# Kernel optimization log

Hardware: AMD Instinct MI355X
Metric: run time of the kernel (lower is better)

The kernel has to match this reference:

```python
import jax, jax.numpy as jnp
import numpy as np
from jax import lax

B, C, H, W = 64, 512, 14, 14
HEAD_DIM = 32
NUM_HEADS = C // HEAD_DIM
HIDDEN = int(C * 4.0)
EPS = 1e-5
LS_INIT = 1e-5


def setup_inputs() -> dict:
    key = jax.random.key(0)
    ks = jax.random.split(key, 16)
    d = {}
    d['x'] = jax.random.normal(ks[0], (B, C, H, W), dtype=jnp.float32)
    # shared BatchNorm2d(dim) (inference-mode, running stats)
    d['bn_g'] = 1.0 + 0.1 * jax.random.normal(ks[1], (C,), dtype=jnp.float32)
    d['bn_b'] = 0.1 * jax.random.normal(ks[2], (C,), dtype=jnp.float32)
    d['bn_m'] = 0.1 * jax.random.normal(ks[3], (C,), dtype=jnp.float32)
    d['bn_v'] = jax.random.uniform(ks[4], (C,), minval=0.5, maxval=1.5, dtype=jnp.float32)
    # MHSA params (qkv_bias=False)
    d['qkv_w'] = 0.02 * jax.random.normal(ks[5], (3 * C, C), dtype=jnp.float32)
    d['proj_w'] = 0.02 * jax.random.normal(ks[6], (C, C), dtype=jnp.float32)
    d['proj_b'] = jnp.zeros((C,), dtype=jnp.float32)
    # ConvFFN: depthwise 7x7 (groups=C, no bias) -> BN -> 1x1 -> GELU -> 1x1
    d['dw_w'] = 0.02 * jax.random.normal(ks[7], (C, 1, 7, 7), dtype=jnp.float32)
    d['fbn_g'] = 1.0 + 0.1 * jax.random.normal(ks[8], (C,), dtype=jnp.float32)
    d['fbn_b'] = 0.1 * jax.random.normal(ks[9], (C,), dtype=jnp.float32)
    d['fbn_m'] = 0.1 * jax.random.normal(ks[10], (C,), dtype=jnp.float32)
    d['fbn_v'] = jax.random.uniform(ks[11], (C,), minval=0.5, maxval=1.5, dtype=jnp.float32)
    d['fc1_w'] = 0.02 * jax.random.normal(ks[12], (HIDDEN, C), dtype=jnp.float32)
    d['fc1_b'] = jnp.zeros((HIDDEN,), dtype=jnp.float32)
    d['fc2_w'] = 0.02 * jax.random.normal(ks[13], (C, HIDDEN), dtype=jnp.float32)
    d['fc2_b'] = jnp.zeros((C,), dtype=jnp.float32)
    # layer scale params, shape (C,1,1)
    d['ls1'] = LS_INIT * jnp.ones((C, 1, 1), dtype=jnp.float32)
    d['ls2'] = LS_INIT * jnp.ones((C, 1, 1), dtype=jnp.float32)
    return d


def _bn2d(x, g, b, m, v):
    # inference BatchNorm2d over channel dim of NCHW
    inv = g * lax.rsqrt(v + EPS)
    return x * inv[None, :, None, None] + (b - m * inv)[None, :, None, None]


def _mhsa(x, qkv_w, proj_w, proj_b):
    b, c, h, w = x.shape
    n = h * w
    xt = x.reshape(b, c, n).transpose(0, 2, 1)              # [B,N,C]
    qkv = xt @ qkv_w.T                                       # [B,N,3C]
    qkv = qkv.reshape(b, n, 3, NUM_HEADS, HEAD_DIM).transpose(2, 0, 3, 1, 4)
    q, k, v = qkv[0], qkv[1], qkv[2]                         # [B,h,N,d]
    scale = HEAD_DIM ** -0.5
    attn = jax.nn.softmax(jnp.einsum('bhnd,bhmd->bhnm', q * scale, k), axis=-1)
    o = jnp.einsum('bhnm,bhmd->bhnd', attn, v)               # [B,h,N,d]
    o = o.transpose(0, 2, 1, 3).reshape(b, n, c)             # [B,N,C]
    o = o @ proj_w.T + proj_b
    return o.transpose(0, 2, 1).reshape(b, c, h, w)


def _convffn(x, dw_w, fbn_g, fbn_b, fbn_m, fbn_v, fc1_w, fc1_b, fc2_w, fc2_b):
    y = lax.conv_general_dilated(x, dw_w, window_strides=(1, 1),
                                 padding=[(3, 3), (3, 3)],
                                 feature_group_count=C,
                                 dimension_numbers=('NCHW', 'OIHW', 'NCHW'))
    y = _bn2d(y, fbn_g, fbn_b, fbn_m, fbn_v)
    y = jnp.einsum('bchw,oc->bohw', y, fc1_w) + fc1_b[None, :, None, None]
    y = jax.nn.gelu(y, approximate=False)
    y = jnp.einsum('bchw,oc->bohw', y, fc2_w) + fc2_b[None, :, None, None]
    return y


def reference(x, bn_g, bn_b, bn_m, bn_v, qkv_w, proj_w, proj_b,
              dw_w, fbn_g, fbn_b, fbn_m, fbn_v, fc1_w, fc1_b, fc2_w, fc2_b,
              ls1, ls2):
    xn = _bn2d(x, bn_g, bn_b, bn_m, bn_v)
    x = x + ls1[None] * _mhsa(xn, qkv_w, proj_w, proj_b)
    xn = _bn2d(x, bn_g, bn_b, bn_m, bn_v)
    x = x + ls2[None] * _convffn(xn, dw_w, fbn_g, fbn_b, fbn_m, fbn_v,
                                 fc1_w, fc1_b, fc2_w, fc2_b)
    return x
```

## Files before the change

### kernel.cpp

```cpp
#include <hip/hip_runtime.h>
#include <hip/hip_bf16.h>
#include <hip/hip_fp8.h>
#include <stdint.h>

#define NTOK 196
#define NB   64
#define CCH  512
#define HID  2048
#define MTOT (NB * NTOK)

typedef __attribute__((ext_vector_type(8))) short  short8v;
typedef __attribute__((ext_vector_type(4))) float  float4v;
typedef __attribute__((ext_vector_type(2))) int    int2v;


__device__ __forceinline__ void mfma16x16(float4v& d, short8v a, short8v b) {
  asm("v_mfma_f32_16x16x32_bf16 %0, %1, %2, %0" : "+v"(d) : "v"(a), "v"(b));
}

__device__ __forceinline__ void mfma_fp8(float4v& d, int2v a, int2v b) {
  asm("v_mfma_f32_16x16x32_fp8_fp8 %0, %1, %2, %0" : "+v"(d) : "v"(a), "v"(b));
}

__device__ __forceinline__ void gload_lds16(const void* gsrc, void* ldst) {
  __builtin_amdgcn_global_load_lds(
      (const __attribute__((address_space(1))) unsigned int*)gsrc,
      (__attribute__((address_space(3))) unsigned int*)ldst, 16, 0, 0);
}

__device__ __forceinline__ int swz4(int r) { return (r ^ (r >> 2)) & 3; }

__device__ __forceinline__ uint8_t to_fp8(float v) {
  return __hip_fp8_e4m3(v).__x;
}


__global__ void prep_consts(const float* __restrict__ bn_g, const float* __restrict__ bn_b,
                            const float* __restrict__ bn_m, const float* __restrict__ bn_v,
                            const float* __restrict__ fbn_g, const float* __restrict__ fbn_b,
                            const float* __restrict__ fbn_m, const float* __restrict__ fbn_v,
                            float* __restrict__ cst) {
  int c = blockIdx.x * blockDim.x + threadIdx.x;
  if (c < CCH) {
    float i1 = bn_g[c] * rsqrtf(bn_v[c] + 1e-5f);
    cst[c] = i1;
    cst[512 + c] = bn_b[c] - bn_m[c] * i1;
    float i2 = fbn_g[c] * rsqrtf(fbn_v[c] + 1e-5f);
    cst[1024 + c] = i2;
    cst[1536 + c] = fbn_b[c] - fbn_m[c] * i2;
  }
}


__global__ void cvt_weights(const float* __restrict__ qkv_w, const float* __restrict__ proj_w,
                            const float* __restrict__ fc1_w, const float* __restrict__ fc2_w,
                            uint8_t* __restrict__ qkvb, uint8_t* __restrict__ projb,
                            uint8_t* __restrict__ fc1b, uint8_t* __restrict__ fc2b) {
  int i4 = blockIdx.x * blockDim.x + threadIdx.x;
  const int nq = 1536 * 512 / 4;
  const int np = 512 * 512 / 4;
  const int n1 = 2048 * 512 / 4;
  const float* src;
  uint8_t* dst;
  int k;
  if (i4 < nq)                { src = qkv_w;  dst = qkvb;  k = i4; }
  else if (i4 < nq + np)      { src = proj_w; dst = projb; k = i4 - nq; }
  else if (i4 < nq + np + n1) { src = fc1_w;  dst = fc1b;  k = i4 - nq - np; }
  else                        { src = fc2_w;  dst = fc2b;  k = i4 - nq - np - n1; }
  float4v v = *(const float4v*)(src + 4 * (size_t)k);
  #pragma unroll
  for (int l = 0; l < 4; ++l) dst[4 * (size_t)k + l] = to_fp8(v[l] * 16.0f);
}


__global__ __launch_bounds__(256) void transpose_x(
    const float* __restrict__ x, uint8_t* __restrict__ xnt8,
    __hip_bfloat16* __restrict__ xt, const float* __restrict__ cst) {
  __shared__ float tile[32][33];
  const int n0 = blockIdx.x * 32;
  const int c0 = blockIdx.y * 32;
  const int b  = blockIdx.z;
  const int j = threadIdx.x & 31, i = threadIdx.x >> 5;
  #pragma unroll
  for (int p = 0; p < 4; ++p) {
    int cc = c0 + i + p * 8;
    int n = n0 + j;
    if (n < NTOK) tile[i + p * 8][j] = x[((size_t)b * CCH + cc) * NTOK + n];
  }
  __syncthreads();
  const float s = cst[c0 + j], t = cst[512 + c0 + j];
  #pragma unroll
  for (int p = 0; p < 4; ++p) {
    int n = n0 + i + p * 8;
    int cc = c0 + j;
    if (n < NTOK) {
      float raw = tile[j][i + p * 8];
      size_t o = ((size_t)b * NTOK + n) * CCH + cc;
      xt[o]   = __float2bfloat16(raw);
      xnt8[o] = to_fp8(raw * s + t);
    }
  }
}


template<int EPI>
__global__ __launch_bounds__(256, 3) void gemm8f(
    const uint8_t* __restrict__ A, const uint8_t* __restrict__ Bw,
    int N, int K, int NY,
    __hip_bfloat16* __restrict__ outb, uint8_t* __restrict__ out8,
    float* __restrict__ outf,
    const float* __restrict__ bias, const float* __restrict__ ls,
    const __hip_bfloat16* __restrict__ resid) {
  __shared__ char lds[49152];
  const int tid  = threadIdx.x;
  const int lane = tid & 63;
  const int wave = tid >> 6;

  const int q    = (int)gridDim.x >> 3;
  const int orig = blockIdx.x;
  const int wgid = (orig & 7) * q + (orig >> 3);
  const int bx = wgid / NY;
  const int by = wgid - bx * NY;

  const int m0 = bx * 128;
  const int n0 = by * 128;
  const int wm = (wave >> 1) * 64;
  const int wn = (wave & 1) * 64;
  const int KT = K >> 6;

  float4v acc[4][4] = {};

  auto stage = [&](int buf, int kt) {
    const int kb = kt * 64;
    char* base = lds + buf * 16384;
    #pragma unroll
    for (int i = 0; i < 2; ++i) {
      int L = i * 4096 + tid * 16;
      int row = L >> 6;
      int lc = ((L >> 4) & 3) ^ swz4(row);
      gload_lds16(A + (size_t)(m0 + row) * K + kb + lc * 16, base + L);
    }
    #pragma unroll
    for (int i = 0; i < 2; ++i) {
      int L = i * 4096 + tid * 16;
      int row = L >> 6;
      int lc = ((L >> 4) & 3) ^ swz4(row);
      gload_lds16(Bw + (size_t)(n0 + row) * K + kb + lc * 16, base + 8192 + L);
    }
  };

  auto compute = [&](int buf) {
    const char* bA = lds + buf * 16384;
    const char* bB = bA + 8192;
    const int g = lane >> 4;
    #pragma unroll
    for (int t = 0; t < 2; ++t) {
      int2v av[4], bv[4];
      #pragma unroll
      for (int f = 0; f < 4; ++f) {
        int row = wm + f * 16 + (lane & 15);
        int c16 = ((t << 1) | (g >> 1)) ^ swz4(row);
        av[f] = *(const int2v*)(bA + row * 64 + c16 * 16 + (g & 1) * 8);
      }
      #pragma unroll
      for (int j = 0; j < 4; ++j) {
        int row = wn + j * 16 + (lane & 15);
        int c16 = ((t << 1) | (g >> 1)) ^ swz4(row);
        bv[j] = *(const int2v*)(bB + row * 64 + c16 * 16 + (g & 1) * 8);
      }
      #pragma unroll
      for (int i = 0; i < 4; ++i)
        #pragma unroll
        for (int j = 0; j < 4; ++j)
          mfma_fp8(acc[i][j], av[i], bv[j]);
    }
  };

  stage(0, 0);
  stage(1, 1);
  int cur = 0;
  for (int kt = 0; kt < KT - 1; ++kt) {
    asm volatile("s_waitcnt vmcnt(4)" ::: "memory");
    __builtin_amdgcn_s_barrier();
    __builtin_amdgcn_sched_barrier(0);
    if (kt + 2 < KT) {
      int s = cur + 2; if (s >= 3) s -= 3;
      stage(s, kt + 2);
    }
    compute(cur);
    ++cur; if (cur == 3) cur = 0;
  }
  asm volatile("s_waitcnt vmcnt(0)" ::: "memory");
  __builtin_amdgcn_s_barrier();
  __builtin_amdgcn_sched_barrier(0);
  compute(cur);
  asm volatile("s_nop 7\n\ts_nop 7");

  const float RS = 0.0625f;

  if (EPI == 0 || EPI == 2) {
    #pragma unroll
    for (int i = 0; i < 4; ++i)
      #pragma unroll
      for (int j = 0; j < 4; ++j)
        #pragma unroll
        for (int r = 0; r < 4; ++r) {
          int m = m0 + wm + i * 16 + ((lane >> 4) << 2) + r;
          int n = n0 + wn + j * 16 + (lane & 15);
          float v = acc[i][j][r] * RS;
          if (EPI == 0) {
            outb[(size_t)m * N + n] = __float2bfloat16(v);
          } else {
            float z = v + bias[n];
            float g2 = z / (1.0f + __expf(-1.702f * z));
            out8[(size_t)m * N + n] = to_fp8(g2);
          }
        }
  } else if (EPI == 1) {
    #pragma unroll
    for (int i = 0; i < 4; ++i)
      #pragma unroll
      for (int j = 0; j < 4; ++j)
        #pragma unroll
        for (int r = 0; r < 4; ++r) {
          int m = m0 + wm + i * 16 + ((lane >> 4) << 2) + r;
          int n = n0 + wn + j * 16 + (lane & 15);
          float v = acc[i][j][r] * RS + bias[n];
          v = __bfloat162float(resid[(size_t)m * CCH + n]) + ls[n] * v;
          outb[(size_t)m * CCH + n] = __float2bfloat16(v);
        }
  } else {
    float* LT = (float*)lds;
    #pragma unroll 1
    for (int hh = 0; hh < 2; ++hh) {
      __syncthreads();
      if ((wn >> 6) == hh) {
        #pragma unroll
        for (int i = 0; i < 4; ++i)
          #pragma unroll
          for (int j = 0; j < 4; ++j)
            #pragma unroll
            for (int r = 0; r < 4; ++r) {
              int ml = wm + i * 16 + ((lane >> 4) << 2) + r;
              int nl = j * 16 + (lane & 15);
              int n = n0 + wn + nl;
              float v = acc[i][j][r] * RS + bias[n];
              v = __bfloat162float(resid[(size_t)(m0 + ml) * CCH + n]) + ls[n] * v;
              LT[nl * 129 + ml] = v;
            }
      }
      __syncthreads();
      {
        int ml0 = lane << 1;
        int mg = m0 + ml0;
        int bb0 = mg / NTOK;
        int tt0 = mg - bb0 * NTOK;
        int bb1 = (mg + 1) / NTOK;
        int tt1 = (mg + 1) - bb1 * NTOK;
        size_t base0 = (size_t)bb0 * (CCH * NTOK) + tt0;
        size_t base1 = (size_t)bb1 * (CCH * NTOK) + tt1;
        #pragma unroll
        for (int u = 0; u < 16; ++u) {
          int cr = wave * 16 + u;
          int cg = n0 + hh * 64 + cr;
          float v0 = LT[cr * 129 + ml0];
          float v1 = LT[cr * 129 + ml0 + 1];
          outf[base0 + (size_t)cg * NTOK] = v0;
          outf[base1 + (size_t)cg * NTOK] = v1;
        }
      }
    }
  }
}


__global__ __launch_bounds__(256, 2) void attn_kernel(
    const __hip_bfloat16* __restrict__ qkv, uint8_t* __restrict__ o_t8) {
  __shared__ char sQ[208 * 64];
  __shared__ char sK[224 * 64];
  __shared__ char sV[32 * 448];
  __shared__ char sP[4][16 * 472];
  const int tid  = threadIdx.x;
  const int lane = tid & 63;
  const int wave = tid >> 6;
  const int b = blockIdx.x >> 4;
  const int h = blockIdx.x & 15;
  const size_t qbase = (size_t)b * NTOK * 1536 + h * 32;

  {
    uint32_t* z = (uint32_t*)sQ;
    for (int i = tid; i < (208 * 64) / 4; i += 256) z[i] = 0u;
    z = (uint32_t*)sK;
    for (int i = tid; i < (224 * 64) / 4; i += 256) z[i] = 0u;
    z = (uint32_t*)sV;
    for (int i = tid; i < (32 * 448) / 4; i += 256) z[i] = 0u;
  }
  __syncthreads();

  for (int p = tid; p < NTOK * 4; p += 256) {
    int row = p >> 2, c = p & 3;
    const __hip_bfloat16* src = qkv + qbase + (size_t)row * 1536 + c * 8;
    short8v q = *(const short8v*)(src);
    short8v k = *(const short8v*)(src + 512);
    short8v v = *(const short8v*)(src + 1024);
    int pc = c ^ swz4(row);
    *(short8v*)(sQ + row * 64 + pc * 16) = q;
    *(short8v*)(sK + row * 64 + pc * 16) = k;
    #pragma unroll
    for (int j = 0; j < 8; ++j) {
      int d = c * 8 + j;
      int ch = (row >> 3) ^ swz4(d);
      *(uint16_t*)(sV + d * 448 + ch * 16 + (row & 7) * 2) = (uint16_t)v[j];
    }
  }
  __syncthreads();

  const float scale = 0.17677669529663687f;
  char* Pw = sP[wave];

  for (int mt = wave; mt < 13; mt += 4) {
    int qrow = mt * 16 + (lane & 15);
    int pcq = (lane >> 4) ^ swz4(qrow);
    short8v aq = *(const short8v*)(sQ + qrow * 64 + pcq * 16);

    float4v s[14];
    #pragma unroll
    for (int nt = 0; nt < 14; ++nt) {
      int krow = nt * 16 + (lane & 15);
      int pck = (lane >> 4) ^ swz4(krow);
      short8v bk = *(const short8v*)(sK + krow * 64 + pck * 16);
      s[nt] = float4v{0.f, 0.f, 0.f, 0.f};
      mfma16x16(s[nt], aq, bk);
    }
    asm volatile("s_nop 7\n\ts_nop 7");

    float mx[4] = {-INFINITY, -INFINITY, -INFINITY, -INFINITY};
    #pragma unroll
    for (int nt = 0; nt < 14; ++nt) {
      bool valid = (nt * 16 + (lane & 15)) < NTOK;
      #pragma unroll
      for (int r = 0; r < 4; ++r) {
        float v = valid ? s[nt][r] * scale : -INFINITY;
        s[nt][r] = v;
        mx[r] = fmaxf(mx[r], v);
      }
    }
    #pragma unroll
    for (int off = 1; off < 16; off <<= 1) {
      #pragma unroll
      for (int r = 0; r < 4; ++r) mx[r] = fmaxf(mx[r], __shfl_xor(mx[r], off));
    }
    float sum[4] = {0.f, 0.f, 0.f, 0.f};
    #pragma unroll
    for (int nt = 0; nt < 14; ++nt) {
      #pragma unroll
      for (int r = 0; r < 4; ++r) {
        float e = __expf(s[nt][r] - mx[r]);
        s[nt][r] = e;
        sum[r] += e;
      }
    }
    #pragma unroll
    for (int off = 1; off < 16; off <<= 1) {
      #pragma unroll
      for (int r = 0; r < 4; ++r) sum[r] += __shfl_xor(sum[r], off);
    }
    float rs[4];
    #pragma unroll
    for (int r = 0; r < 4; ++r) rs[r] = 1.0f / sum[r];

    #pragma unroll
    for (int nt = 0; nt < 14; ++nt) {
      int col = nt * 16 + (lane & 15);
      #pragma unroll
      for (int r = 0; r < 4; ++r) {
        int prow = ((lane >> 4) << 2) + r;
        *(__hip_bfloat16*)(Pw + prow * 472 + col * 2) = __float2bfloat16(s[nt][r] * rs[r]);
      }
    }

    float4v o0 = float4v{0.f, 0.f, 0.f, 0.f};
    float4v o1 = float4v{0.f, 0.f, 0.f, 0.f};
    #pragma unroll
    for (int ks = 0; ks < 7; ++ks) {
      short8v pa = *(const short8v*)(Pw + (lane & 15) * 472 + ks * 64 + ((lane >> 4) << 4));
      int kc = ks * 4 + (lane >> 4);
      int d0 = (lane & 15);
      int d1 = 16 + (lane & 15);
      short8v v0 = *(const short8v*)(sV + d0 * 448 + ((kc ^ swz4(d0)) << 4));
      short8v v1 = *(const short8v*)(sV + d1 * 448 + ((kc ^ swz4(d1)) << 4));
      mfma16x16(o0, pa, v0);
      mfma16x16(o1, pa, v1);
    }
    asm volatile("s_nop 7\n\ts_nop 7");

    #pragma unroll
    for (int r = 0; r < 4; ++r) {
      int trow = mt * 16 + ((lane >> 4) << 2) + r;
      if (trow < NTOK) {
        size_t ob = ((size_t)b * NTOK + trow) * CCH + h * 32 + (lane & 15);
        o_t8[ob] = to_fp8(o0[r]);
        o_t8[ob + 16] = to_fp8(o1[r]);
      }
    }
  }
}


__global__ __launch_bounds__(448) void dwconv_tm(
    const __hip_bfloat16* __restrict__ x1t, const float* __restrict__ dw_w,
    const float* __restrict__ cst, uint8_t* __restrict__ yt8) {
  __shared__ float img[196][32];
  __shared__ float wgt[49][32];
  const int tid = threadIdx.x;
  const int b  = blockIdx.x >> 4;
  const int cb = (blockIdx.x & 15) * 32;
  const int c  = tid & 31;
  const int gc = cb + c;
  const float s = cst[gc], t0 = cst[512 + gc];
  #pragma unroll
  for (int k = 0; k < 14; ++k) {
    int p = (tid >> 5) + k * 14;
    img[p][c] = __bfloat162float(x1t[((size_t)b * NTOK + p) * CCH + gc]) * s + t0;
  }
  for (int i = tid; i < 49 * 32; i += 448) {
    int tap = i >> 5, cc = i & 31;
    wgt[tap][cc] = dw_w[(cb + cc) * 49 + tap];
  }
  __syncthreads();

  const int px = tid >> 5;
  float out[14];
  #pragma unroll
  for (int i = 0; i < 14; ++i) out[i] = 0.f;
  #pragma unroll 1
  for (int row = 0; row < 14; ++row) {
    float v[7];
    #pragma unroll
    for (int dx = 0; dx < 7; ++dx) {
      int ix = px + dx - 3;
      v[dx] = ((unsigned)ix < 14u) ? img[row * 14 + ix][c] : 0.f;
    }
    #pragma unroll
    for (int kk = 0; kk < 7; ++kk) {
      int py = row + 3 - kk;
      if (py >= 0 && py < 14) {
        float hsum = 0.f;
        #pragma unroll
        for (int dx = 0; dx < 7; ++dx) hsum = fmaf(v[dx], wgt[kk * 7 + dx][c], hsum);
        out[py] += hsum;
      }
    }
  }
  const float fs = cst[1024 + gc], ft = cst[1536 + gc];
  #pragma unroll
  for (int py = 0; py < 14; ++py)
    yt8[((size_t)b * NTOK + py * 14 + px) * CCH + gc] = to_fp8(out[py] * fs + ft);
}


extern "C" void kernel_launch(void* const* d_in, const int* in_sizes, int n_in,
                              void* d_out, int out_size, void* d_ws, size_t ws_size,
                              hipStream_t stream) {
  const float* x      = (const float*)d_in[0];
  const float* bn_g   = (const float*)d_in[1];
  const float* bn_b   = (const float*)d_in[2];
  const float* bn_m   = (const float*)d_in[3];
  const float* bn_v   = (const float*)d_in[4];
  const float* qkv_w  = (const float*)d_in[5];
  const float* proj_w = (const float*)d_in[6];
  const float* proj_b = (const float*)d_in[7];
  const float* dw_w   = (const float*)d_in[8];
  const float* fbn_g  = (const float*)d_in[9];
  const float* fbn_b  = (const float*)d_in[10];
  const float* fbn_m  = (const float*)d_in[11];
  const float* fbn_v  = (const float*)d_in[12];
  const float* fc1_w  = (const float*)d_in[13];
  const float* fc1_b  = (const float*)d_in[14];
  const float* fc2_w  = (const float*)d_in[15];
  const float* fc2_b  = (const float*)d_in[16];
  const float* ls1    = (const float*)d_in[17];
  const float* ls2    = (const float*)d_in[18];

  char* ws = (char*)d_ws;
  float* cst             = (float*)ws;
  uint8_t* qkvb8         = (uint8_t*)(ws + 32768);
  uint8_t* projb8        = (uint8_t*)(ws + 819200);
  uint8_t* fc1b8         = (uint8_t*)(ws + 1081344);
  uint8_t* fc2b8         = (uint8_t*)(ws + 2129920);
  uint8_t* xnt8          = (uint8_t*)(ws + 3178496);
  __hip_bfloat16* xt     = (__hip_bfloat16*)(ws + 9601024);
  __hip_bfloat16* qkvt   = (__hip_bfloat16*)(ws + 22446080);
  uint8_t* ot8           = (uint8_t*)(ws + 60981248);
  __hip_bfloat16* x1t    = (__hip_bfloat16*)(ws + 67403776);
  uint8_t* yt8           = (uint8_t*)(ws + 80248832);
  uint8_t* h8            = (uint8_t*)(ws + 3178496);

  prep_consts<<<dim3(2), dim3(256), 0, stream>>>(bn_g, bn_b, bn_m, bn_v,
                                                 fbn_g, fbn_b, fbn_m, fbn_v, cst);
  cvt_weights<<<dim3(3072), dim3(256), 0, stream>>>(qkv_w, proj_w, fc1_w, fc2_w,
                                                    qkvb8, projb8, fc1b8, fc2b8);
  transpose_x<<<dim3(7, 16, 64), dim3(256), 0, stream>>>(x, xnt8, xt, cst);
  gemm8f<0><<<dim3(1176), dim3(256), 0, stream>>>(xnt8, qkvb8, 1536, 512, 12,
                                                  qkvt, nullptr, nullptr, nullptr, nullptr, nullptr);
  attn_kernel<<<dim3(1024), dim3(256), 0, stream>>>(qkvt, ot8);
  gemm8f<1><<<dim3(392), dim3(256), 0, stream>>>(ot8, projb8, 512, 512, 4,
                                                 x1t, nullptr, nullptr, proj_b, ls1, xt);
  dwconv_tm<<<dim3(1024), dim3(448), 0, stream>>>(x1t, dw_w, cst, yt8);
  gemm8f<2><<<dim3(1568), dim3(256), 0, stream>>>(yt8, fc1b8, 2048, 512, 16,
                                                  nullptr, h8, nullptr, fc1_b, nullptr, nullptr);
  gemm8f<3><<<dim3(392), dim3(256), 0, stream>>>(h8, fc2b8, 512, 2048, 4,
                                                 nullptr, nullptr, (float*)d_out, fc2_b, ls2, x1t);
}
```

Measured before the change: 218.7 us.

## Store QKV as FP8 in head-major layout and run attention with FP8 MFMA

The QKV GEMM epilogue now writes FP8 values scattered into a per-(q/k/v, head, batch) contiguous layout instead of row-major bf16. The attention kernel loads these compact tiles directly, zeroes only the padding, and uses fp8 MFMAs for both QK^T and PV. Softmax normalization is deferred to the output, and occupancy is raised to 3 blocks per SM. This halves QKV traffic and LDS use but adds FP8 quantization error on Q, K, V and unnormalized probabilities, and scattered byte stores in the GEMM epilogue.

```diff
diff --git a/kernel.cpp b/kernel.cpp
--- a/kernel.cpp
+++ b/kernel.cpp
@@ -13,10 +13,6 @@
 typedef __attribute__((ext_vector_type(4))) float  float4v;
 typedef __attribute__((ext_vector_type(2))) int    int2v;
 
-
-__device__ __forceinline__ void mfma16x16(float4v& d, short8v a, short8v b) {
-  asm("v_mfma_f32_16x16x32_bf16 %0, %1, %2, %0" : "+v"(d) : "v"(a), "v"(b));
-}
 
 __device__ __forceinline__ void mfma_fp8(float4v& d, int2v a, int2v b) {
   asm("v_mfma_f32_16x16x32_fp8_fp8 %0, %1, %2, %0" : "+v"(d) : "v"(a), "v"(b));
@@ -198,7 +194,7 @@
 
   const float RS = 0.0625f;
 
-  if (EPI == 0 || EPI == 2) {
+  if (EPI == 0) {
     #pragma unroll
     for (int i = 0; i < 4; ++i)
       #pragma unroll
@@ -207,14 +203,23 @@
         for (int r = 0; r < 4; ++r) {
           int m = m0 + wm + i * 16 + ((lane >> 4) << 2) + r;
           int n = n0 + wn + j * 16 + (lane & 15);
-          float v = acc[i][j][r] * RS;
-          if (EPI == 0) {
-            outb[(size_t)m * N + n] = __float2bfloat16(v);
-          } else {
-            float z = v + bias[n];
-            float g2 = z / (1.0f + __expf(-1.702f * z));
-            out8[(size_t)m * N + n] = to_fp8(g2);
-          }
+          int bb = m / NTOK, tok = m - bb * NTOK;
+          int sel = n >> 9, hh = (n >> 5) & 15, d = n & 31;
+          out8[(((size_t)(sel * 16 + hh) * NB + bb) * NTOK + tok) * 32 + d] =
+              to_fp8(acc[i][j][r] * RS);
+        }
+  } else if (EPI == 2) {
+    #pragma unroll
+    for (int i = 0; i < 4; ++i)
+      #pragma unroll
+      for (int j = 0; j < 4; ++j)
+        #pragma unroll
+        for (int r = 0; r < 4; ++r) {
+          int m = m0 + wm + i * 16 + ((lane >> 4) << 2) + r;
+          int n = n0 + wn + j * 16 + (lane & 15);
+          float z = acc[i][j][r] * RS + bias[n];
+          float g2 = z / (1.0f + __expf(-1.702f * z));
+          out8[(size_t)m * N + n] = to_fp8(g2);
         }
   } else if (EPI == 1) {
     #pragma unroll
@@ -274,63 +279,66 @@
 }
 
 
-__global__ __launch_bounds__(256, 2) void attn_kernel(
-    const __hip_bfloat16* __restrict__ qkv, uint8_t* __restrict__ o_t8) {
-  __shared__ char sQ[208 * 64];
-  __shared__ char sK[224 * 64];
-  __shared__ char sV[32 * 448];
-  __shared__ char sP[4][16 * 472];
+__global__ __launch_bounds__(256, 3) void attn_kernel(
+    const uint8_t* __restrict__ qkv8, uint8_t* __restrict__ o_t8) {
+  __shared__ char sQ[208 * 48];
+  __shared__ char sK[224 * 48];
+  __shared__ char sV[32 * 240];
+  __shared__ char sP[4][16 * 232];
   const int tid  = threadIdx.x;
   const int lane = tid & 63;
   const int wave = tid >> 6;
   const int b = blockIdx.x >> 4;
   const int h = blockIdx.x & 15;
-  const size_t qbase = (size_t)b * NTOK * 1536 + h * 32;
-
-  {
-    uint32_t* z = (uint32_t*)sQ;
-    for (int i = tid; i < (208 * 64) / 4; i += 256) z[i] = 0u;
-    z = (uint32_t*)sK;
-    for (int i = tid; i < (224 * 64) / 4; i += 256) z[i] = 0u;
-    z = (uint32_t*)sV;
-    for (int i = tid; i < (32 * 448) / 4; i += 256) z[i] = 0u;
-  }
-  __syncthreads();
-
-  for (int p = tid; p < NTOK * 4; p += 256) {
-    int row = p >> 2, c = p & 3;
-    const __hip_bfloat16* src = qkv + qbase + (size_t)row * 1536 + c * 8;
-    short8v q = *(const short8v*)(src);
-    short8v k = *(const short8v*)(src + 512);
-    short8v v = *(const short8v*)(src + 1024);
-    int pc = c ^ swz4(row);
-    *(short8v*)(sQ + row * 64 + pc * 16) = q;
-    *(short8v*)(sK + row * 64 + pc * 16) = k;
-    #pragma unroll
-    for (int j = 0; j < 8; ++j) {
-      int d = c * 8 + j;
-      int ch = (row >> 3) ^ swz4(d);
-      *(uint16_t*)(sV + d * 448 + ch * 16 + (row & 7) * 2) = (uint16_t)v[j];
-    }
+  const size_t CHB = 6272;
+  const uint8_t* Qg = qkv8 + ((size_t)(0 * 16 + h) * NB + b) * CHB;
+  const uint8_t* Kg = qkv8 + ((size_t)(1 * 16 + h) * NB + b) * CHB;
+  const uint8_t* Vg = qkv8 + ((size_t)(2 * 16 + h) * NB + b) * CHB;
+
+  for (int i = tid; i < 144; i += 256) {
+    int r = i / 12, w = i % 12;
+    ((uint32_t*)(sQ + (196 + r) * 48))[w] = 0u;
+  }
+  for (int i = tid; i < 336; i += 256) {
+    int r = i / 12, w = i % 12;
+    ((uint32_t*)(sK + (196 + r) * 48))[w] = 0u;
+  }
+  for (int i = tid; i < 352; i += 256) {
+    int d = i / 11, w = i % 11;
+    ((uint32_t*)(sV + d * 240 + 196))[w] = 0u;
+  }
+
+  for (int c = tid; c < 392; c += 256) {
+    int row = c >> 1, hf = c & 1;
+    uint4 vq = *(const uint4*)(Qg + c * 16);
+    *(uint4*)(sQ + row * 48 + hf * 16) = vq;
+    uint4 vk = *(const uint4*)(Kg + c * 16);
+    *(uint4*)(sK + row * 48 + hf * 16) = vk;
+  }
+  for (int u = tid; u < 784; u += 256) {
+    int row = u >> 2, d0 = (u & 3) * 8;
+    uint64_t w = *(const uint64_t*)(Vg + (size_t)u * 8);
+    #pragma unroll
+    for (int e = 0; e < 8; ++e)
+      sV[(d0 + e) * 240 + row] = (char)(w >> (8 * e));
   }
   __syncthreads();
 
   const float scale = 0.17677669529663687f;
   char* Pw = sP[wave];
+  const int g = lane >> 4;
 
   for (int mt = wave; mt < 13; mt += 4) {
     int qrow = mt * 16 + (lane & 15);
-    int pcq = (lane >> 4) ^ swz4(qrow);
-    short8v aq = *(const short8v*)(sQ + qrow * 64 + pcq * 16);
+    int2v aq = *(const int2v*)(sQ + qrow * 48 + g * 8);
 
     float4v s[14];
     #pragma unroll
     for (int nt = 0; nt < 14; ++nt) {
       int krow = nt * 16 + (lane & 15);
-      int pck = (lane >> 4) ^ swz4(krow);
-      short8v bk = *(const short8v*)(sK + krow * 64 + pck * 16);
+      int2v bk = *(const int2v*)(sK + krow * 48 + g * 8);
       s[nt] = float4v{0.f, 0.f, 0.f, 0.f};
-      mfma16x16(s[nt], aq, bk);
+      mfma_fp8(s[nt], aq, bk);
     }
     asm volatile("s_nop 7\n\ts_nop 7");
 
@@ -375,7 +383,7 @@
       #pragma unroll
       for (int r = 0; r < 4; ++r) {
         int prow = ((lane >> 4) << 2) + r;
-        *(__hip_bfloat16*)(Pw + prow * 472 + col * 2) = __float2bfloat16(s[nt][r] * rs[r]);
+        *(uint8_t*)(Pw + prow * 232 + col) = to_fp8(s[nt][r]);
       }
     }
 
@@ -383,14 +391,11 @@
     float4v o1 = float4v{0.f, 0.f, 0.f, 0.f};
     #pragma unroll
     for (int ks = 0; ks < 7; ++ks) {
-      short8v pa = *(const short8v*)(Pw + (lane & 15) * 472 + ks * 64 + ((lane >> 4) << 4));
-      int kc = ks * 4 + (lane >> 4);
-      int d0 = (lane & 15);
-      int d1 = 16 + (lane & 15);
-      short8v v0 = *(const short8v*)(sV + d0 * 448 + ((kc ^ swz4(d0)) << 4));
-      short8v v1 = *(const short8v*)(sV + d1 * 448 + ((kc ^ swz4(d1)) << 4));
-      mfma16x16(o0, pa, v0);
-      mfma16x16(o1, pa, v1);
+      int2v pa = *(const int2v*)(Pw + (lane & 15) * 232 + ks * 32 + g * 8);
+      int2v v0 = *(const int2v*)(sV + (lane & 15) * 240 + ks * 32 + g * 8);
+      int2v v1 = *(const int2v*)(sV + (16 + (lane & 15)) * 240 + ks * 32 + g * 8);
+      mfma_fp8(o0, pa, v0);
+      mfma_fp8(o1, pa, v1);
     }
     asm volatile("s_nop 7\n\ts_nop 7");
 
@@ -399,8 +404,8 @@
       int trow = mt * 16 + ((lane >> 4) << 2) + r;
       if (trow < NTOK) {
         size_t ob = ((size_t)b * NTOK + trow) * CCH + h * 32 + (lane & 15);
-        o_t8[ob] = to_fp8(o0[r]);
-        o_t8[ob + 16] = to_fp8(o1[r]);
+        o_t8[ob] = to_fp8(o0[r] * rs[r]);
+        o_t8[ob + 16] = to_fp8(o1[r] * rs[r]);
       }
     }
   }
@@ -490,7 +495,7 @@
   uint8_t* fc2b8         = (uint8_t*)(ws + 2129920);
   uint8_t* xnt8          = (uint8_t*)(ws + 3178496);
   __hip_bfloat16* xt     = (__hip_bfloat16*)(ws + 9601024);
-  __hip_bfloat16* qkvt   = (__hip_bfloat16*)(ws + 22446080);
+  uint8_t* qkv8          = (uint8_t*)(ws + 22446080);
   uint8_t* ot8           = (uint8_t*)(ws + 60981248);
   __hip_bfloat16* x1t    = (__hip_bfloat16*)(ws + 67403776);
   uint8_t* yt8           = (uint8_t*)(ws + 80248832);
@@ -502,8 +507,8 @@
                                                     qkvb8, projb8, fc1b8, fc2b8);
   transpose_x<<<dim3(7, 16, 64), dim3(256), 0, stream>>>(x, xnt8, xt, cst);
   gemm8f<0><<<dim3(1176), dim3(256), 0, stream>>>(xnt8, qkvb8, 1536, 512, 12,
-                                                  qkvt, nullptr, nullptr, nullptr, nullptr, nullptr);
-  attn_kernel<<<dim3(1024), dim3(256), 0, stream>>>(qkvt, ot8);
+                                                  nullptr, qkv8, nullptr, nullptr, nullptr, nullptr);
+  attn_kernel<<<dim3(1024), dim3(256), 0, stream>>>(qkv8, ot8);
   gemm8f<1><<<dim3(392), dim3(256), 0, stream>>>(ot8, projb8, 512, 512, 4,
                                                  x1t, nullptr, nullptr, proj_b, ls1, xt);
   dwconv_tm<<<dim3(1024), dim3(448), 0, stream>>>(x1t, dw_w, cst, yt8);
```

Result: faster. 205.6 us (-6.0%).
